# Performance work log

Measured on AMD Instinct MI355X. Metric: run time of the kernel, lower is better.

## Reference

```python
import jax, jax.numpy as jnp
import numpy as np

B, C, H, W = 8, 64, 32, 32
NEG = 256
TEMP = 2.0
FACTOR = 0.8
EPS = 1e-8


def setup_inputs() -> dict:
    key = jax.random.key(0)
    k1, k2, k3, k4 = jax.random.split(key, 4)
    views_1 = jax.random.normal(k1, (B, C, H, W), dtype=jnp.float32)
    views_2 = jax.random.normal(k2, (B, C, H, W), dtype=jnp.float32)
    img = jax.random.uniform(k3, (1, 3, H, W), dtype=jnp.float32)
    neg_idx = jax.random.randint(k4, (B, 2, H * W, NEG), 0, H, dtype=jnp.int32)
    return {"views_1": views_1, "views_2": views_2, "img": img, "neg_idx": neg_idx}


def _forward(views_1, views_2, img, neg_idx):
    hw = H * W
    height = jnp.arange(hw) // W
    width = jnp.arange(hw) % W
    coords = jnp.stack([height, width]).astype(jnp.float32)  # [2, hw]
    img0 = img[0]  # [3, H, W]; original uses img[0] for EVERY batch element
    euc_norm = jnp.sqrt(jnp.asarray((H - 1) ** 2 + (W - 1) ** 2, jnp.float32))
    sqrt3 = jnp.sqrt(jnp.asarray(3.0, jnp.float32))

    center = img0[:, height, width]  # [3, hw]

    def per_sample(z1, z2, nidx):
        # nidx: [2, hw, neg]
        nf = nidx.astype(jnp.float32)
        # torch.norm with no dim => scalar Frobenius norm over [2, neg] per pixel
        d = coords[:, :, None] - nf  # [2, hw, neg]
        euc = jnp.sqrt(jnp.sum(d * d, axis=(0, 2))) / euc_norm  # [hw]
        negs = img0[:, nidx[0], nidx[1]]  # [3, hw, neg]
        rd = center[:, :, None] - negs
        rgb = jnp.sqrt(jnp.sum(rd * rd, axis=(0, 2))) / sqrt3  # [hw]
        weight = euc * FACTOR + rgb * (1.0 - FACTOR)  # [hw], constant across neg

        z1v = z1.reshape(C, hw)  # [c, hw]
        pn = z2[:, nidx[0], nidx[1]]  # [c, hw, neg]
        dot = jnp.einsum('cp,cpn->pn', z1v, pn)  # [hw, neg]
        z1sq = jnp.sum(z1v * z1v, axis=0)  # [hw]
        z1n = jnp.sqrt(z1sq)
        pnn = jnp.sqrt(jnp.sum(pn * pn, axis=0))  # [hw, neg]
        cos = dot / jnp.maximum(z1n[:, None] * pnn, EPS)  # [hw, neg]
        cos0 = z1sq / jnp.maximum(z1sq, EPS)  # [hw] (self-similarity ~ 1)

        sim_neg = jnp.minimum(jnp.abs(cos * weight[:, None]), 1.0)  # [hw, neg]
        sim0 = jnp.minimum(jnp.abs(cos0), 1.0)  # [hw]
        sim = jnp.concatenate(
            [jnp.mean(sim0)[None], jnp.mean(sim_neg, axis=0) / TEMP]
        )  # [neg+1]

        # BCELoss with target = [1, 0, ..., 0]; torch clamps log terms at -100
        logp = jnp.maximum(jnp.log(sim[0]), -100.0)
        log1m = jnp.maximum(jnp.log1p(-sim[1:]), -100.0)
        bce = -(logp + jnp.sum(log1m)) / (NEG + 1)
        return bce, sim

    bce, sims = jax.vmap(per_sample)(views_1, views_2, neg_idx)
    loss = jnp.mean(bce)
    sim_all = jnp.sum(sims, axis=0)
    return (loss, sim_all[0] / B, jnp.sum(sim_all[1:]) / NEG * TEMP / B)


def reference(views_1, views_2, img, neg_idx):
    return _forward(views_1, views_2, img, neg_idx)
```

## Files before the change

kernel.cpp:

```cpp
#include <hip/hip_runtime.h>
#include <math.h>

#define BB 8
#define CC 64
#define HH 32
#define WW 32
#define HW 1024
#define NEGN 256
#define TEMP 2.0f
#define FACTOR 0.8f
#define EPSF 1e-8f

typedef short bf16x8 __attribute__((ext_vector_type(8)));
typedef float f32x4  __attribute__((ext_vector_type(4)));

__device__ inline unsigned short f2bf(float f) {
    unsigned u = __float_as_uint(f);
    u += 0x7FFFu + ((u >> 16) & 1u);
    return (unsigned short)(u >> 16);
}


__global__ __launch_bounds__(256) void prep_z2(
    const float* __restrict__ z2,
    unsigned short* __restrict__ z2t,
    float* __restrict__ normq_ws)
{
    __shared__ float ctile[64 * 16];

    const int t   = threadIdx.x;
    const int blk = blockIdx.x;
    const int b   = blk >> 6;
    const int q0  = (blk & 63) * 16;

    #pragma unroll
    for (int i = 0; i < 4; ++i) {
        const int idx = t + 256 * i;
        const int c = idx >> 4, row = idx & 15;
        ctile[idx] = z2[((size_t)(b * CC + c)) * HW + q0 + row];
    }
    __syncthreads();

    if (t < 16) {
        float s = 0.f;
        #pragma unroll
        for (int c = 0; c < CC; ++c) { const float v = ctile[c * 16 + t]; s += v * v; }
        normq_ws[b * 1024 + q0 + t] = sqrtf(s);
    }

    unsigned short* dst = z2t + ((size_t)(b * 1024) + q0) * 64;
    ushort4 pk;
    const int o = 4 * t;
    pk.x = f2bf(ctile[((o + 0) & 63) * 16 + ((o + 0) >> 6)]);
    pk.y = f2bf(ctile[((o + 1) & 63) * 16 + ((o + 1) >> 6)]);
    pk.z = f2bf(ctile[((o + 2) & 63) * 16 + ((o + 2) >> 6)]);
    pk.w = f2bf(ctile[((o + 3) & 63) * 16 + ((o + 3) >> 6)]);
    *reinterpret_cast<ushort4*>(dst + o) = pk;
}

__global__ __launch_bounds__(256, 2) void gemm_fused(
    const float* __restrict__ z1,
    const float* __restrict__ img,
    const int*   __restrict__ nidx,
    const unsigned short* __restrict__ z2t,
    const float* __restrict__ normq_ws,
    float* __restrict__ simPart,
    float* __restrict__ sim0Part)
{
    __shared__ float Dt_s[16 * HW];
    __shared__ float imgs_l[3 * HW];
    __shared__ float z1sq_s[16];

    const int t    = threadIdx.x;
    const int blk  = blockIdx.x;
    const int b    = blk >> 6;
    const int p0   = (blk & 63) * 16;
    const int wave = t >> 6;
    const int lane = t & 63;
    const int ln15 = lane & 15;
    const int lg   = lane >> 4;

    const int p_b = t >> 4;
    const int tn  = t & 15;
    const size_t nbase = ((size_t)(b * 2) * HW + p0 + p_b) * NEGN;
    const int2* __restrict__ nr = reinterpret_cast<const int2*>(nidx + nbase);
    const int2* __restrict__ nc =
        reinterpret_cast<const int2*>(nidx + nbase + (size_t)HW * NEGN);
    int2 rrv[8], ccv[8];
    #pragma unroll
    for (int j = 0; j < 8; ++j) {
        rrv[j] = nr[tn + 16 * j];
        ccv[j] = nc[tn + 16 * j];
    }

    {
        const float4* __restrict__ imgf4 = reinterpret_cast<const float4*>(img);
        float4* imgs4 = reinterpret_cast<float4*>(imgs_l);
        #pragma unroll
        for (int j = 0; j < 3; ++j) imgs4[t + 256 * j] = imgf4[t + 256 * j];
    }

    const int qw = wave * 256;
    float pnv[16];
    #pragma unroll
    for (int tile = 0; tile < 16; ++tile)
        pnv[tile] = normq_ws[b * 1024 + qw + tile * 16 + ln15];

    const float* __restrict__ z1p = z1 + (size_t)(b * CC) * HW + p0 + ln15;
    float av0[8], av1[8];
    #pragma unroll
    for (int j = 0; j < 8; ++j) {
        av0[j] = z1p[(size_t)(lg * 8 + j) * HW];
        av1[j] = z1p[(size_t)(32 + lg * 8 + j) * HW];
    }
    float zsq = 0.f;
    #pragma unroll
    for (int j = 0; j < 8; ++j) zsq += av0[j] * av0[j];
    #pragma unroll
    for (int j = 0; j < 8; ++j) zsq += av1[j] * av1[j];
    zsq += __shfl_xor(zsq, 16);
    zsq += __shfl_xor(zsq, 32);
    const float z1n_mine = sqrtf(zsq);
    float z1n_row[4];
    #pragma unroll
    for (int i = 0; i < 4; ++i) z1n_row[i] = __shfl(z1n_mine, lg * 4 + i);

    bf16x8 a0, a1;
    #pragma unroll
    for (int j = 0; j < 8; ++j) {
        a0[j] = (short)f2bf(av0[j]);
        a1[j] = (short)f2bf(av1[j]);
    }
    if (wave == 0 && lane < 16) z1sq_s[lane] = zsq;

    __syncthreads();

    #pragma unroll 4
    for (int tile = 0; tile < 16; ++tile) {
        const int q0t = qw + tile * 16;
        const unsigned short* brow =
            z2t + ((size_t)(b * 1024) + q0t + ln15) * 64 + lg * 8;
        const bf16x8 b0 = *reinterpret_cast<const bf16x8*>(brow);
        const bf16x8 b1 = *reinterpret_cast<const bf16x8*>(brow + 32);
        f32x4 acc = {0.f, 0.f, 0.f, 0.f};
        acc = __builtin_amdgcn_mfma_f32_16x16x32_bf16(a0, b0, acc, 0, 0, 0);
        acc = __builtin_amdgcn_mfma_f32_16x16x32_bf16(a1, b1, acc, 0, 0, 0);
        #pragma unroll
        for (int i = 0; i < 4; ++i) {
            const int row = lg * 4 + i;
            Dt_s[row * HW + q0t + ln15] =
                acc[i] / fmaxf(z1n_row[i] * pnv[tile], EPSF);
        }
    }

    const int pg = p0 + p_b;
    const float cen0 = imgs_l[pg], cen1 = imgs_l[HW + pg], cen2 = imgs_l[2 * HW + pg];
    const float hp = (float)(pg >> 5), wp = (float)(pg & 31);

    int qv[16];
    float se = 0.f, sr = 0.f;
    #pragma unroll
    for (int j = 0; j < 8; ++j) {
        {
            const int q = rrv[j].x * WW + ccv[j].x; qv[2 * j] = q;
            const float dh = hp - (float)rrv[j].x, dw = wp - (float)ccv[j].x;
            se += dh * dh + dw * dw;
            const float d0 = cen0 - imgs_l[q];
            const float d1 = cen1 - imgs_l[HW + q];
            const float d2 = cen2 - imgs_l[2 * HW + q];
            sr += d0 * d0 + d1 * d1 + d2 * d2;
        }
        {
            const int q = rrv[j].y * WW + ccv[j].y; qv[2 * j + 1] = q;
            const float dh = hp - (float)rrv[j].y, dw = wp - (float)ccv[j].y;
            se += dh * dh + dw * dw;
            const float d0 = cen0 - imgs_l[q];
            const float d1 = cen1 - imgs_l[HW + q];
            const float d2 = cen2 - imgs_l[2 * HW + q];
            sr += d0 * d0 + d1 * d1 + d2 * d2;
        }
    }
    #pragma unroll
    for (int off = 8; off; off >>= 1) {
        se += __shfl_xor(se, off);
        sr += __shfl_xor(sr, off);
    }
    const float euc_norm = sqrtf((float)((HH - 1) * (HH - 1) + (WW - 1) * (WW - 1)));
    const float weight = sqrtf(se) / euc_norm * FACTOR +
                         sqrtf(sr) / sqrtf(3.0f) * (1.0f - FACTOR);

    __syncthreads();

    float2 sv[8];
    #pragma unroll
    for (int j = 0; j < 8; ++j) {
        const float c0 = Dt_s[p_b * HW + qv[2 * j]];
        const float c1 = Dt_s[p_b * HW + qv[2 * j + 1]];
        sv[j].x = fminf(fabsf(c0 * weight), 1.0f);
        sv[j].y = fminf(fabsf(c1 * weight), 1.0f);
    }
    __syncthreads();

    float2* simpart2 = reinterpret_cast<float2*>(Dt_s);
    #pragma unroll
    for (int j = 0; j < 8; ++j)
        simpart2[p_b * (NEGN / 2) + tn + 16 * j] = sv[j];
    __syncthreads();

    float s = 0.f;
    #pragma unroll
    for (int pp = 0; pp < 16; ++pp) s += Dt_s[pp * NEGN + t];
    simPart[(size_t)blk * NEGN + t] = s;

    if (t == 0) {
        float s0 = 0.f;
        #pragma unroll
        for (int pp = 0; pp < 16; ++pp)
            s0 += fminf(fabsf(z1sq_s[pp] / fmaxf(z1sq_s[pp], EPSF)), 1.0f);
        sim0Part[blk] = s0;
    }
}

__global__ __launch_bounds__(256) void reduce_out(
    const float* __restrict__ simPart,
    const float* __restrict__ sim0Part,
    float* __restrict__ out)
{
    const int b = blockIdx.x;
    const int t = threadIdx.x;

    float a = 0.f;
    #pragma unroll 8
    for (int pblk = 0; pblk < 64; ++pblk)
        a += simPart[((size_t)(b * 64 + pblk)) * NEGN + t];

    const float s = a * (1.0f / HW) * (1.0f / TEMP);
    float ssum = s;
    float lsum = fmaxf(log1pf(-s), -100.0f);

    __shared__ float rs[4], rl[4];
    __shared__ float s0sh;
    #pragma unroll
    for (int off = 32; off; off >>= 1) {
        ssum += __shfl_down(ssum, off);
        lsum += __shfl_down(lsum, off);
    }
    if ((t & 63) == 0) { rs[t >> 6] = ssum; rl[t >> 6] = lsum; }

    if (t < 64) {
        float v = sim0Part[b * 64 + t];
        #pragma unroll
        for (int off = 32; off; off >>= 1) v += __shfl_xor(v, off);
        if (t == 0) s0sh = v * (1.0f / HW);
    }
    __syncthreads();

    if (t == 0) {
        const float S = rs[0] + rs[1] + rs[2] + rs[3];
        const float L = rl[0] + rl[1] + rl[2] + rl[3];
        const float s0 = s0sh;
        const float logp = fmaxf(logf(s0), -100.0f);
        atomicAdd(out + 0, -(logp + L) / ((float)(NEGN + 1) * (float)BB));
        atomicAdd(out + 1, s0 / (float)BB);
        atomicAdd(out + 2, S / (float)NEGN * TEMP / (float)BB);
    }
}

extern "C" void kernel_launch(void* const* d_in, const int* in_sizes, int n_in,
                              void* d_out, int out_size, void* d_ws, size_t ws_size,
                              hipStream_t stream) {
    const float* v1   = (const float*)d_in[0];
    const float* v2   = (const float*)d_in[1];
    const float* img  = (const float*)d_in[2];
    const int*   nidx = (const int*)  d_in[3];

    float*    simPart  = (float*)d_ws;
    float*    sim0Part = simPart + 512 * NEGN;
    float*    normq_ws = sim0Part + 512;
    unsigned short* z2t = (unsigned short*)(normq_ws + 8192);

    prep_z2<<<512, 256, 0, stream>>>(v2, z2t, normq_ws);
    gemm_fused<<<512, 256, 0, stream>>>(v1, img, nidx, z2t, normq_ws,
                                        simPart, sim0Part);
    reduce_out<<<BB, 256, 0, stream>>>(simPart, sim0Part, (float*)d_out);
}
```

Baseline: 90.87 us.

## Fuse z2 transpose and norm computation into the main GEMM kernel

Removes the separate prep_z2 kernel that transposed z2 to bf16 and computed its per-pixel norms. The fused kernel now reads fp32 z2 directly in channel-major layout, computes the squared norms with shuffles and converts to bf16 in registers before each MFMA. This saves one launch and the workspace round trip. In exchange, every one of the 64 blocks per batch re-reads all of z2 with strided fp32 loads (twice the bytes of bf16) and redoes the norm and conversion work.

```diff
diff --git a/kernel.cpp b/kernel.cpp
--- a/kernel.cpp
+++ b/kernel.cpp
@@ -21,49 +21,11 @@
 }
 
 
-__global__ __launch_bounds__(256) void prep_z2(
-    const float* __restrict__ z2,
-    unsigned short* __restrict__ z2t,
-    float* __restrict__ normq_ws)
-{
-    __shared__ float ctile[64 * 16];
-
-    const int t   = threadIdx.x;
-    const int blk = blockIdx.x;
-    const int b   = blk >> 6;
-    const int q0  = (blk & 63) * 16;
-
-    #pragma unroll
-    for (int i = 0; i < 4; ++i) {
-        const int idx = t + 256 * i;
-        const int c = idx >> 4, row = idx & 15;
-        ctile[idx] = z2[((size_t)(b * CC + c)) * HW + q0 + row];
-    }
-    __syncthreads();
-
-    if (t < 16) {
-        float s = 0.f;
-        #pragma unroll
-        for (int c = 0; c < CC; ++c) { const float v = ctile[c * 16 + t]; s += v * v; }
-        normq_ws[b * 1024 + q0 + t] = sqrtf(s);
-    }
-
-    unsigned short* dst = z2t + ((size_t)(b * 1024) + q0) * 64;
-    ushort4 pk;
-    const int o = 4 * t;
-    pk.x = f2bf(ctile[((o + 0) & 63) * 16 + ((o + 0) >> 6)]);
-    pk.y = f2bf(ctile[((o + 1) & 63) * 16 + ((o + 1) >> 6)]);
-    pk.z = f2bf(ctile[((o + 2) & 63) * 16 + ((o + 2) >> 6)]);
-    pk.w = f2bf(ctile[((o + 3) & 63) * 16 + ((o + 3) >> 6)]);
-    *reinterpret_cast<ushort4*>(dst + o) = pk;
-}
-
 __global__ __launch_bounds__(256, 2) void gemm_fused(
     const float* __restrict__ z1,
+    const float* __restrict__ z2,
     const float* __restrict__ img,
     const int*   __restrict__ nidx,
-    const unsigned short* __restrict__ z2t,
-    const float* __restrict__ normq_ws,
     float* __restrict__ simPart,
     float* __restrict__ sim0Part)
 {
@@ -100,12 +62,6 @@
         for (int j = 0; j < 3; ++j) imgs4[t + 256 * j] = imgf4[t + 256 * j];
     }
 
-    const int qw = wave * 256;
-    float pnv[16];
-    #pragma unroll
-    for (int tile = 0; tile < 16; ++tile)
-        pnv[tile] = normq_ws[b * 1024 + qw + tile * 16 + ln15];
-
     const float* __restrict__ z1p = z1 + (size_t)(b * CC) * HW + p0 + ln15;
     float av0[8], av1[8];
     #pragma unroll
@@ -135,13 +91,33 @@
 
     __syncthreads();
 
+    const int qw = wave * 256;
+    const float* __restrict__ z2p = z2 + (size_t)(b * CC) * HW;
     #pragma unroll 4
     for (int tile = 0; tile < 16; ++tile) {
-        const int q0t = qw + tile * 16;
-        const unsigned short* brow =
-            z2t + ((size_t)(b * 1024) + q0t + ln15) * 64 + lg * 8;
-        const bf16x8 b0 = *reinterpret_cast<const bf16x8*>(brow);
-        const bf16x8 b1 = *reinterpret_cast<const bf16x8*>(brow + 32);
+        const int q0t  = qw + tile * 16;
+        const int qrow = q0t + ln15;
+        float bv0[8], bv1[8];
+        #pragma unroll
+        for (int j = 0; j < 8; ++j) {
+            bv0[j] = z2p[(size_t)(lg * 8 + j) * HW + qrow];
+            bv1[j] = z2p[(size_t)(32 + lg * 8 + j) * HW + qrow];
+        }
+        float qsq = 0.f;
+        #pragma unroll
+        for (int j = 0; j < 8; ++j) qsq += bv0[j] * bv0[j];
+        #pragma unroll
+        for (int j = 0; j < 8; ++j) qsq += bv1[j] * bv1[j];
+        qsq += __shfl_xor(qsq, 16);
+        qsq += __shfl_xor(qsq, 32);
+        const float pn = sqrtf(qsq);
+
+        bf16x8 b0, b1;
+        #pragma unroll
+        for (int j = 0; j < 8; ++j) {
+            b0[j] = (short)f2bf(bv0[j]);
+            b1[j] = (short)f2bf(bv1[j]);
+        }
         f32x4 acc = {0.f, 0.f, 0.f, 0.f};
         acc = __builtin_amdgcn_mfma_f32_16x16x32_bf16(a0, b0, acc, 0, 0, 0);
         acc = __builtin_amdgcn_mfma_f32_16x16x32_bf16(a1, b1, acc, 0, 0, 0);
@@ -149,7 +125,7 @@
         for (int i = 0; i < 4; ++i) {
             const int row = lg * 4 + i;
             Dt_s[row * HW + q0t + ln15] =
-                acc[i] / fmaxf(z1n_row[i] * pnv[tile], EPSF);
+                acc[i] / fmaxf(z1n_row[i] * pn, EPSF);
         }
     }
 
@@ -274,13 +250,9 @@
     const float* img  = (const float*)d_in[2];
     const int*   nidx = (const int*)  d_in[3];
 
-    float*    simPart  = (float*)d_ws;
-    float*    sim0Part = simPart + 512 * NEGN;
-    float*    normq_ws = sim0Part + 512;
-    unsigned short* z2t = (unsigned short*)(normq_ws + 8192);
-
-    prep_z2<<<512, 256, 0, stream>>>(v2, z2t, normq_ws);
-    gemm_fused<<<512, 256, 0, stream>>>(v1, img, nidx, z2t, normq_ws,
-                                        simPart, sim0Part);
+    float* simPart  = (float*)d_ws;
+    float* sim0Part = simPart + 512 * NEGN;
+
+    gemm_fused<<<512, 256, 0, stream>>>(v1, v2, img, nidx, simPart, sim0Part);
     reduce_out<<<BB, 256, 0, stream>>>(simPart, sim0Part, (float*)d_out);
 }
```

After: 91.66 us. About the same (+0.9%).

## Halve pixels per block, store image in bf16 LDS, double grid for occupancy

Applied to the files above, without the earlier changes.

Each block now handles 8 pixels instead of 16, so the grid doubles to 1024 blocks. LDS per block drops: the cosine tile is halved and the image copy is stored as bf16, which allows 4 blocks per CU. The 16x16 MFMA tiles are still computed in full, but only the first 8 rows are written, so half the matrix work is wasted. Storing the image in bf16 lowers the precision of the RGB distance weight, and the reduce kernel is updated to sum 128 partials per batch.

```diff
diff --git a/kernel.cpp b/kernel.cpp
--- a/kernel.cpp
+++ b/kernel.cpp
@@ -19,6 +19,9 @@
     u += 0x7FFFu + ((u >> 16) & 1u);
     return (unsigned short)(u >> 16);
 }
+__device__ inline float bf2f(unsigned short h) {
+    return __uint_as_float((unsigned)h << 16);
+}
 
 
 __global__ __launch_bounds__(256) void prep_z2(
@@ -58,7 +61,7 @@
     *reinterpret_cast<ushort4*>(dst + o) = pk;
 }
 
-__global__ __launch_bounds__(256, 2) void gemm_fused(
+__global__ __launch_bounds__(256, 4) void gemm_fused(
     const float* __restrict__ z1,
     const float* __restrict__ img,
     const int*   __restrict__ nidx,
@@ -67,46 +70,46 @@
     float* __restrict__ simPart,
     float* __restrict__ sim0Part)
 {
-    __shared__ float Dt_s[16 * HW];
-    __shared__ float imgs_l[3 * HW];
-    __shared__ float z1sq_s[16];
+    __shared__ float Dt_s[8 * HW];
+    __shared__ unsigned short imgs_h[3 * HW];
+    __shared__ float z1sq_s[8];
 
     const int t    = threadIdx.x;
     const int blk  = blockIdx.x;
-    const int b    = blk >> 6;
-    const int p0   = (blk & 63) * 16;
+    const int b    = blk >> 7;
+    const int p0   = (blk & 127) * 8;
     const int wave = t >> 6;
     const int lane = t & 63;
     const int ln15 = lane & 15;
     const int lg   = lane >> 4;
-
-    const int p_b = t >> 4;
-    const int tn  = t & 15;
+    const int row8 = ln15 & 7;
+
+    const int p_b    = t >> 5;
+    const int lane32 = t & 31;
     const size_t nbase = ((size_t)(b * 2) * HW + p0 + p_b) * NEGN;
     const int2* __restrict__ nr = reinterpret_cast<const int2*>(nidx + nbase);
     const int2* __restrict__ nc =
         reinterpret_cast<const int2*>(nidx + nbase + (size_t)HW * NEGN);
-    int2 rrv[8], ccv[8];
-    #pragma unroll
-    for (int j = 0; j < 8; ++j) {
-        rrv[j] = nr[tn + 16 * j];
-        ccv[j] = nc[tn + 16 * j];
+    int2 rrv[4], ccv[4];
+    #pragma unroll
+    for (int j = 0; j < 4; ++j) {
+        rrv[j] = nr[lane32 + 32 * j];
+        ccv[j] = nc[lane32 + 32 * j];
     }
 
     {
         const float4* __restrict__ imgf4 = reinterpret_cast<const float4*>(img);
-        float4* imgs4 = reinterpret_cast<float4*>(imgs_l);
-        #pragma unroll
-        for (int j = 0; j < 3; ++j) imgs4[t + 256 * j] = imgf4[t + 256 * j];
-    }
-
-    const int qw = wave * 256;
-    float pnv[16];
-    #pragma unroll
-    for (int tile = 0; tile < 16; ++tile)
-        pnv[tile] = normq_ws[b * 1024 + qw + tile * 16 + ln15];
-
-    const float* __restrict__ z1p = z1 + (size_t)(b * CC) * HW + p0 + ln15;
+        ushort4* imgs4 = reinterpret_cast<ushort4*>(imgs_h);
+        #pragma unroll
+        for (int j = 0; j < 3; ++j) {
+            const float4 v = imgf4[t + 256 * j];
+            ushort4 h;
+            h.x = f2bf(v.x); h.y = f2bf(v.y); h.z = f2bf(v.z); h.w = f2bf(v.w);
+            imgs4[t + 256 * j] = h;
+        }
+    }
+
+    const float* __restrict__ z1p = z1 + (size_t)(b * CC) * HW + p0 + row8;
     float av0[8], av1[8];
     #pragma unroll
     for (int j = 0; j < 8; ++j) {
@@ -131,7 +134,13 @@
         a0[j] = (short)f2bf(av0[j]);
         a1[j] = (short)f2bf(av1[j]);
     }
-    if (wave == 0 && lane < 16) z1sq_s[lane] = zsq;
+    if (wave == 0 && lane < 8) z1sq_s[lane] = zsq;
+
+    const int qw = wave * 256;
+    float pnv[16];
+    #pragma unroll
+    for (int tile = 0; tile < 16; ++tile)
+        pnv[tile] = normq_ws[b * 1024 + qw + tile * 16 + ln15];
 
     __syncthreads();
 
@@ -145,43 +154,47 @@
         f32x4 acc = {0.f, 0.f, 0.f, 0.f};
         acc = __builtin_amdgcn_mfma_f32_16x16x32_bf16(a0, b0, acc, 0, 0, 0);
         acc = __builtin_amdgcn_mfma_f32_16x16x32_bf16(a1, b1, acc, 0, 0, 0);
-        #pragma unroll
-        for (int i = 0; i < 4; ++i) {
-            const int row = lg * 4 + i;
-            Dt_s[row * HW + q0t + ln15] =
-                acc[i] / fmaxf(z1n_row[i] * pnv[tile], EPSF);
+        if (lg < 2) {
+            #pragma unroll
+            for (int i = 0; i < 4; ++i) {
+                const int row = lg * 4 + i;
+                Dt_s[row * HW + q0t + ln15] =
+                    acc[i] / fmaxf(z1n_row[i] * pnv[tile], EPSF);
+            }
         }
     }
 
     const int pg = p0 + p_b;
-    const float cen0 = imgs_l[pg], cen1 = imgs_l[HW + pg], cen2 = imgs_l[2 * HW + pg];
+    const float cen0 = bf2f(imgs_h[pg]);
+    const float cen1 = bf2f(imgs_h[HW + pg]);
+    const float cen2 = bf2f(imgs_h[2 * HW + pg]);
     const float hp = (float)(pg >> 5), wp = (float)(pg & 31);
 
-    int qv[16];
+    int qv[8];
     float se = 0.f, sr = 0.f;
     #pragma unroll
-    for (int j = 0; j < 8; ++j) {
+    for (int j = 0; j < 4; ++j) {
         {
             const int q = rrv[j].x * WW + ccv[j].x; qv[2 * j] = q;
             const float dh = hp - (float)rrv[j].x, dw = wp - (float)ccv[j].x;
             se += dh * dh + dw * dw;
-            const float d0 = cen0 - imgs_l[q];
-            const float d1 = cen1 - imgs_l[HW + q];
-            const float d2 = cen2 - imgs_l[2 * HW + q];
+            const float d0 = cen0 - bf2f(imgs_h[q]);
+            const float d1 = cen1 - bf2f(imgs_h[HW + q]);
+            const float d2 = cen2 - bf2f(imgs_h[2 * HW + q]);
             sr += d0 * d0 + d1 * d1 + d2 * d2;
         }
         {
             const int q = rrv[j].y * WW + ccv[j].y; qv[2 * j + 1] = q;
             const float dh = hp - (float)rrv[j].y, dw = wp - (float)ccv[j].y;
             se += dh * dh + dw * dw;
-            const float d0 = cen0 - imgs_l[q];
-            const float d1 = cen1 - imgs_l[HW + q];
-            const float d2 = cen2 - imgs_l[2 * HW + q];
+            const float d0 = cen0 - bf2f(imgs_h[q]);
+            const float d1 = cen1 - bf2f(imgs_h[HW + q]);
+            const float d2 = cen2 - bf2f(imgs_h[2 * HW + q]);
             sr += d0 * d0 + d1 * d1 + d2 * d2;
         }
     }
     #pragma unroll
-    for (int off = 8; off; off >>= 1) {
+    for (int off = 16; off; off >>= 1) {
         se += __shfl_xor(se, off);
         sr += __shfl_xor(sr, off);
     }
@@ -191,31 +204,29 @@
 
     __syncthreads();
 
-    float2 sv[8];
-    #pragma unroll
-    for (int j = 0; j < 8; ++j) {
-        const float c0 = Dt_s[p_b * HW + qv[2 * j]];
-        const float c1 = Dt_s[p_b * HW + qv[2 * j + 1]];
-        sv[j].x = fminf(fabsf(c0 * weight), 1.0f);
-        sv[j].y = fminf(fabsf(c1 * weight), 1.0f);
-    }
-    __syncthreads();
-
-    float2* simpart2 = reinterpret_cast<float2*>(Dt_s);
-    #pragma unroll
-    for (int j = 0; j < 8; ++j)
-        simpart2[p_b * (NEGN / 2) + tn + 16 * j] = sv[j];
+    float sv[8];
+    #pragma unroll
+    for (int e = 0; e < 8; ++e)
+        sv[e] = fminf(fabsf(Dt_s[p_b * HW + qv[e]] * weight), 1.0f);
+    __syncthreads();
+
+    float* simpart = Dt_s;
+    #pragma unroll
+    for (int j = 0; j < 4; ++j) {
+        simpart[p_b * NEGN + lane32 + 32 * (2 * j)]     = sv[2 * j];
+        simpart[p_b * NEGN + lane32 + 32 * (2 * j + 1)] = sv[2 * j + 1];
+    }
     __syncthreads();
 
     float s = 0.f;
     #pragma unroll
-    for (int pp = 0; pp < 16; ++pp) s += Dt_s[pp * NEGN + t];
+    for (int pp = 0; pp < 8; ++pp) s += simpart[pp * NEGN + t];
     simPart[(size_t)blk * NEGN + t] = s;
 
     if (t == 0) {
         float s0 = 0.f;
         #pragma unroll
-        for (int pp = 0; pp < 16; ++pp)
+        for (int pp = 0; pp < 8; ++pp)
             s0 += fminf(fabsf(z1sq_s[pp] / fmaxf(z1sq_s[pp], EPSF)), 1.0f);
         sim0Part[blk] = s0;
     }
@@ -231,8 +242,8 @@
 
     float a = 0.f;
     #pragma unroll 8
-    for (int pblk = 0; pblk < 64; ++pblk)
-        a += simPart[((size_t)(b * 64 + pblk)) * NEGN + t];
+    for (int pblk = 0; pblk < 128; ++pblk)
+        a += simPart[((size_t)(b * 128 + pblk)) * NEGN + t];
 
     const float s = a * (1.0f / HW) * (1.0f / TEMP);
     float ssum = s;
@@ -248,7 +259,7 @@
     if ((t & 63) == 0) { rs[t >> 6] = ssum; rl[t >> 6] = lsum; }
 
     if (t < 64) {
-        float v = sim0Part[b * 64 + t];
+        float v = sim0Part[b * 128 + t] + sim0Part[b * 128 + 64 + t];
         #pragma unroll
         for (int off = 32; off; off >>= 1) v += __shfl_xor(v, off);
         if (t == 0) s0sh = v * (1.0f / HW);
@@ -275,12 +286,12 @@
     const int*   nidx = (const int*)  d_in[3];
 
     float*    simPart  = (float*)d_ws;
-    float*    sim0Part = simPart + 512 * NEGN;
-    float*    normq_ws = sim0Part + 512;
+    float*    sim0Part = simPart + 1024 * NEGN;
+    float*    normq_ws = sim0Part + 1024;
     unsigned short* z2t = (unsigned short*)(normq_ws + 8192);
 
     prep_z2<<<512, 256, 0, stream>>>(v2, z2t, normq_ws);
-    gemm_fused<<<512, 256, 0, stream>>>(v1, img, nidx, z2t, normq_ws,
-                                        simPart, sim0Part);
+    gemm_fused<<<1024, 256, 0, stream>>>(v1, img, nidx, z2t, normq_ws,
+                                         simPart, sim0Part);
     reduce_out<<<BB, 256, 0, stream>>>(simPart, sim0Part, (float*)d_out);
 }
```

After: 98.91 us. 8.8% more time.
